# Performance work log

Hardware: AMD Instinct MI355X
Metric: run time of the kernel (lower is better)

Reference implementation:

```python
import jax, jax.numpy as jnp
import numpy as np

B, S, E = 2, 2048, 2048
H, HKV, D = 32, 8, 64  # n_heads, n_kv_heads, head_dim


def _rope(x, cos, sin):
    # x: [B,S,h,D]; cos/sin: [1,S,1,D//2]. Complex rotate on (even,odd) pairs.
    xp = x.reshape(*x.shape[:-1], D // 2, 2)
    x0, x1 = xp[..., 0], xp[..., 1]
    r0 = x0 * cos - x1 * sin
    r1 = x0 * sin + x1 * cos
    return jnp.stack([r0, r1], axis=-1).reshape(x.shape)


def setup_inputs() -> dict:
    key = jax.random.key(0)
    ks = jax.random.split(key, 8)
    sc = 0.02
    # real RoPE frequencies (theta=10000) for realism
    inv = 1.0 / (10000.0 ** (np.arange(0, D, 2, dtype=np.float32) / D))
    t = np.arange(S, dtype=np.float32)
    ang = np.outer(t, inv)  # [S, D/2]
    return {
        "x": jax.random.normal(ks[0], (B, S, E), jnp.float32),
        "start_pos": 0,
        "freqs_cos": jnp.asarray(np.cos(ang))[None, :, None, :],
        "freqs_sin": jnp.asarray(np.sin(ang))[None, :, None, :],
        "wq": jax.random.normal(ks[1], (E, H * D), jnp.float32) * sc,
        "wk": jax.random.normal(ks[2], (E, HKV * D), jnp.float32) * sc,
        "wv": jax.random.normal(ks[3], (E, HKV * D), jnp.float32) * sc,
        "out_w": jax.random.normal(ks[4], (H * D, E), jnp.float32) * sc,
        "out_b": jnp.zeros((E,), jnp.float32),
        "k_cache": jnp.zeros((B, S, HKV, D), jnp.float32),
        "v_cache": jnp.zeros((B, S, HKV, D), jnp.float32),
    }


def reference(x, start_pos, freqs_cos, freqs_sin, wq, wk, wv, out_w, out_b, k_cache, v_cache):
    b, s, _ = x.shape
    q = (x @ wq).reshape(b, s, H, D)
    k = (x @ wk).reshape(b, s, HKV, D)
    v = (x @ wv).reshape(b, s, HKV, D)
    q = _rope(q, freqs_cos[:, :s], freqs_sin[:, :s])
    k = _rope(k, freqs_cos[:, :s], freqs_sin[:, :s])
    # KV-cache append (torch code detaches before writing)
    k_cache = jax.lax.dynamic_update_slice(k_cache, jax.lax.stop_gradient(k), (0, start_pos, 0, 0))
    v_cache = jax.lax.dynamic_update_slice(v_cache, jax.lax.stop_gradient(v), (0, start_pos, 0, 0))
    keys = k_cache[:b, : start_pos + s]    # [b, T, HKV, D]
    values = v_cache[:b, : start_pos + s]
    g = H // HKV
    if g > 1:  # GQA head repeat
        keys = jnp.repeat(keys, g, axis=2)     # [b, T, H, D]
        values = jnp.repeat(values, g, axis=2)
    scores = jnp.einsum("bqhd,bkhd->bhqk", q, keys) / jnp.sqrt(jnp.float32(D))
    att = jax.nn.softmax(scores, axis=-1)  # NOTE: source applies no causal mask
    o = jnp.einsum("bhqk,bkhd->bqhd", att, values).reshape(b, s, H * D)
    return o @ out_w + out_b
```

## Files before the change

kernel.cpp:

```cpp
#include <hip/hip_runtime.h>
#include <math.h>

#define B_    2
#define S_    2048
#define E_    2048
#define H_    32
#define HKV_  8
#define D_    64

typedef __bf16 bf16x8 __attribute__((ext_vector_type(8)));
typedef float  f32x4  __attribute__((ext_vector_type(4)));
typedef float  f32x16 __attribute__((ext_vector_type(16)));
typedef unsigned int u32x2 __attribute__((ext_vector_type(2)));
typedef unsigned int u32x4 __attribute__((ext_vector_type(4)));

#define GPTR(x) ((const __attribute__((address_space(1))) void*)(x))
#define LPTR(x) ((__attribute__((address_space(3))) void*)(x))

#define QK_SCALE_LOG2E 0.18033688011112042f

__global__ __launch_bounds__(256) void convert_kernel(
    const float* __restrict__ in, __bf16* __restrict__ out, int n8)
{
    const int i = blockIdx.x * 256 + threadIdx.x;
    if (i >= n8) return;
    const float4 a = ((const float4*)in)[i * 2];
    const float4 b = ((const float4*)in)[i * 2 + 1];
    bf16x8 o;
    o[0] = (__bf16)a.x; o[1] = (__bf16)a.y; o[2] = (__bf16)a.z; o[3] = (__bf16)a.w;
    o[4] = (__bf16)b.x; o[5] = (__bf16)b.y; o[6] = (__bf16)b.z; o[7] = (__bf16)b.w;
    ((bf16x8*)out)[i] = o;
}

__global__ __launch_bounds__(256) void transpose_convert_all_kernel(
    const float* __restrict__ wq, const float* __restrict__ wk,
    const float* __restrict__ wv, const float* __restrict__ wo,
    __bf16* __restrict__ wT, __bf16* __restrict__ woT)
{
    const float* in; __bf16* out; int N, xb;
    const int x = blockIdx.x;
    if (x < 64)      { in = wq; out = wT;                        N = 2048; xb = x; }
    else if (x < 80) { in = wk; out = wT + (size_t)2048 * 2048;  N = 512;  xb = x - 64; }
    else if (x < 96) { in = wv; out = wT + (size_t)2560 * 2048;  N = 512;  xb = x - 80; }
    else             { in = wo; out = woT;                       N = 2048; xb = x - 96; }
    const int K = 2048;

    __shared__ float tile[32][33];
    const int k0 = blockIdx.y * 32, n0 = xb * 32;
    const int r  = threadIdx.x >> 3;
    const int c4 = (threadIdx.x & 7) * 4;
    const float4 v = *(const float4*)&in[(size_t)(k0 + r) * N + n0 + c4];
    tile[r][c4 + 0] = v.x; tile[r][c4 + 1] = v.y;
    tile[r][c4 + 2] = v.z; tile[r][c4 + 3] = v.w;
    __syncthreads();
    ushort4 o;
    __bf16 h0 = (__bf16)tile[c4 + 0][r]; o.x = __builtin_bit_cast(unsigned short, h0);
    __bf16 h1 = (__bf16)tile[c4 + 1][r]; o.y = __builtin_bit_cast(unsigned short, h1);
    __bf16 h2 = (__bf16)tile[c4 + 2][r]; o.z = __builtin_bit_cast(unsigned short, h2);
    __bf16 h3 = (__bf16)tile[c4 + 3][r]; o.w = __builtin_bit_cast(unsigned short, h3);
    *(ushort4*)&out[(size_t)(n0 + r) * K + k0 + c4] = o;
}

__device__ __forceinline__ void gemm_mfma_body(
    const __bf16* __restrict__ A, const __bf16* __restrict__ Bt,
    int m0, int n0, int K, __bf16* sA, __bf16* sB, f32x4 acc[4][4])
{
    const int t    = threadIdx.x;
    const int w    = t >> 6;
    const int lane = t & 63;
    const int col  = lane & 15;
    const int quad = lane >> 4;
    const int wrow = (w >> 1) * 64;
    const int wcol = (w & 1) * 64;

    const int row0 = t >> 3;
    const int c0   = t & 7;

    for (int k0 = 0; k0 < K; k0 += 64) {
#pragma unroll
        for (int it = 0; it < 4; ++it) {
            const int row  = it * 32 + row0;
            const int csrc = c0 ^ (row & 7);
            __builtin_amdgcn_global_load_lds(
                GPTR(A + (size_t)(m0 + row) * K + k0 + csrc * 8),
                LPTR(sA + (it * 256 + t) * 8), 16, 0, 0);
        }
#pragma unroll
        for (int it = 0; it < 4; ++it) {
            const int row  = it * 32 + row0;
            const int csrc = c0 ^ (row & 7);
            __builtin_amdgcn_global_load_lds(
                GPTR(Bt + (size_t)(n0 + row) * K + k0 + csrc * 8),
                LPTR(sB + (it * 256 + t) * 8), 16, 0, 0);
        }
        __syncthreads();

#pragma unroll
        for (int kk = 0; kk < 2; ++kk) {
            bf16x8 af[4], bfr[4];
#pragma unroll
            for (int i = 0; i < 4; ++i) {
                const int m = wrow + i * 16 + col;
                af[i] = *(const bf16x8*)&sA[m * 64 + (((kk * 4 + quad) ^ (m & 7)) * 8)];
            }
#pragma unroll
            for (int j = 0; j < 4; ++j) {
                const int n = wcol + j * 16 + col;
                bfr[j] = *(const bf16x8*)&sB[n * 64 + (((kk * 4 + quad) ^ (n & 7)) * 8)];
            }
#pragma unroll
            for (int i = 0; i < 4; ++i)
#pragma unroll
                for (int j = 0; j < 4; ++j)
                    acc[i][j] = __builtin_amdgcn_mfma_f32_16x16x32_bf16(
                        af[i], bfr[j], acc[i][j], 0, 0, 0);
        }
        __syncthreads();
    }
}

__global__ __launch_bounds__(256) void gemm_qkv_kernel(
    const __bf16* __restrict__ xb, const __bf16* __restrict__ wT,
    const float* __restrict__ fc, const float* __restrict__ fs,
    __bf16* __restrict__ qb, __bf16* __restrict__ kb, __bf16* __restrict__ vb)
{
    __shared__ __bf16 sA[128 * 64];
    __shared__ __bf16 sB[128 * 64];
    f32x4 acc[4][4];
#pragma unroll
    for (int i = 0; i < 4; ++i)
#pragma unroll
        for (int j = 0; j < 4; ++j) acc[i][j] = (f32x4){0.f, 0.f, 0.f, 0.f};

    const int lin     = blockIdx.y * 24 + blockIdx.x;
    const int logical = (lin & 7) * 96 + (lin >> 3);
    const int bx      = logical % 24;
    const int m0      = (logical / 24) * 128;

    gemm_mfma_body(xb, wT, m0, bx * 128, E_, sA, sB, acc);

    __bf16* Cp; int ldc, nb;
    if (bx < 16)      { Cp = qb; ldc = H_ * D_;   nb = bx * 128; }
    else if (bx < 20) { Cp = kb; ldc = HKV_ * D_; nb = (bx - 16) * 128; }
    else              { Cp = vb; ldc = HKV_ * D_; nb = (bx - 20) * 128; }

    const bool  doRope = (bx < 20);
    const float qsc    = (bx < 16) ? QK_SCALE_LOG2E : 1.0f;

    const int lane = threadIdx.x & 63;
    const int col  = lane & 15;
    const int quad = lane >> 4;
    const int wrow = ((threadIdx.x >> 6) >> 1) * 64;
    const int wcol = ((threadIdx.x >> 6) & 1) * 64;
#pragma unroll
    for (int i = 0; i < 4; ++i)
#pragma unroll
        for (int j = 0; j < 4; ++j)
#pragma unroll
            for (int r = 0; r < 4; ++r) {
                const int m = m0 + wrow + i * 16 + quad * 4 + r;
                const int n = nb + wcol + j * 16 + col;
                float val = acc[i][j][r] * qsc;
                if (doRope) {
                    const int   s    = m & (S_ - 1);
                    const int   pair = (n & 63) >> 1;
                    const float c    = fc[s * 32 + pair];
                    const float sn   = fs[s * 32 + pair];
                    const float oth  = __shfl_xor(val, 1);
                    val = (lane & 1) ? (oth * sn + val * c)
                                     : (val * c - oth * sn);
                }
                Cp[(size_t)m * ldc + n] = (__bf16)val;
            }
}

__global__ __launch_bounds__(256) void gemm_out_kernel(
    const __bf16* __restrict__ ob, const __bf16* __restrict__ woT,
    const float* __restrict__ bias, float* __restrict__ out)
{
    __shared__ __bf16 sA[128 * 64];
    __shared__ __bf16 sB[128 * 64];
    f32x4 acc[4][4];
#pragma unroll
    for (int i = 0; i < 4; ++i)
#pragma unroll
        for (int j = 0; j < 4; ++j) acc[i][j] = (f32x4){0.f, 0.f, 0.f, 0.f};

    const int lin     = blockIdx.y * 16 + blockIdx.x;
    const int logical = (lin & 7) * 64 + (lin >> 3);
    const int n0      = (logical % 16) * 128;
    const int m0      = (logical / 16) * 128;

    gemm_mfma_body(ob, woT, m0, n0, H_ * D_, sA, sB, acc);

    const int lane = threadIdx.x & 63;
    const int col  = lane & 15;
    const int quad = lane >> 4;
    const int wrow = ((threadIdx.x >> 6) >> 1) * 64;
    const int wcol = ((threadIdx.x >> 6) & 1) * 64;
#pragma unroll
    for (int i = 0; i < 4; ++i)
#pragma unroll
        for (int j = 0; j < 4; ++j)
#pragma unroll
            for (int r = 0; r < 4; ++r) {
                const int m = m0 + wrow + i * 16 + quad * 4 + r;
                const int n = n0 + wcol + j * 16 + col;
                out[(size_t)m * E_ + n] = acc[i][j][r] + bias[n];
            }
}

struct StageRegs {
    bf16x8  k0, k1;
    ushort4 va0, vc0, va1, vc1;
};

__device__ __forceinline__ void stage_load(
    StageRegs& r, const __bf16* kbase, const __bf16* vbase, int j0,
    int kkey, int kd, int vkp, int vdg)
{
    const int KSTR = HKV_ * D_;
    const __bf16* kr = kbase + (size_t)(j0 + kkey) * KSTR + kd;
    r.k0 = ((const bf16x8*)kr)[0];
    r.k1 = ((const bf16x8*)kr)[1];
    const __bf16* v0 = vbase + (size_t)(j0 + vkp) * KSTR + vdg;
    r.va0 = *(const ushort4*)(v0);
    r.vc0 = *(const ushort4*)(v0 + KSTR);
    r.va1 = *(const ushort4*)(v0 + 32);
    r.vc1 = *(const ushort4*)(v0 + KSTR + 32);
}

__device__ __forceinline__ void stage_write(
    const StageRegs& r, __bf16 (*sK)[72], __bf16 (*sVT)[72],
    int kkey, int kd, int vkp, int vdg)
{
    *(bf16x8*)&sK[kkey][kd]     = r.k0;
    *(bf16x8*)&sK[kkey][kd + 8] = r.k1;
    *(unsigned int*)&sVT[vdg + 0][vkp]      = ((unsigned)r.vc0.x << 16) | r.va0.x;
    *(unsigned int*)&sVT[vdg + 1][vkp]      = ((unsigned)r.vc0.y << 16) | r.va0.y;
    *(unsigned int*)&sVT[vdg + 2][vkp]      = ((unsigned)r.vc0.z << 16) | r.va0.z;
    *(unsigned int*)&sVT[vdg + 3][vkp]      = ((unsigned)r.vc0.w << 16) | r.va0.w;
    *(unsigned int*)&sVT[vdg + 32 + 0][vkp] = ((unsigned)r.vc1.x << 16) | r.va1.x;
    *(unsigned int*)&sVT[vdg + 32 + 1][vkp] = ((unsigned)r.vc1.y << 16) | r.va1.y;
    *(unsigned int*)&sVT[vdg + 32 + 2][vkp] = ((unsigned)r.vc1.z << 16) | r.va1.z;
    *(unsigned int*)&sVT[vdg + 32 + 3][vkp] = ((unsigned)r.vc1.w << 16) | r.va1.w;
}

__device__ __forceinline__ bf16x8 pack_pa(const f32x16& p, int i0)
{
    unsigned a0, a1, a2, a3;
    asm("v_cvt_pk_bf16_f32 %0, %1, %2" : "=v"(a0) : "v"(p[i0 + 0]), "v"(p[i0 + 1]));
    asm("v_cvt_pk_bf16_f32 %0, %1, %2" : "=v"(a1) : "v"(p[i0 + 2]), "v"(p[i0 + 3]));
    asm("v_cvt_pk_bf16_f32 %0, %1, %2" : "=v"(a2) : "v"(p[i0 + 4]), "v"(p[i0 + 5]));
    asm("v_cvt_pk_bf16_f32 %0, %1, %2" : "=v"(a3) : "v"(p[i0 + 6]), "v"(p[i0 + 7]));
    const u32x2 s02 = __builtin_amdgcn_permlane32_swap(a0, a2, false, false);
    const u32x2 s13 = __builtin_amdgcn_permlane32_swap(a1, a3, false, false);
    return __builtin_bit_cast(bf16x8, (u32x4){s02[0], s13[0], s02[1], s13[1]});
}

__device__ __forceinline__ void attn_tile(
    const __bf16 (*sK)[72], const __bf16 (*sVT)[72],
    const bf16x8* bQ, int lq, int hi,
    f32x16& O0, f32x16& O1, float& lsum)
{
    bf16x8 pa[4];
#pragma unroll
    for (int kb = 0; kb < 2; ++kb) {
        f32x16 p;
#pragma unroll
        for (int i = 0; i < 16; ++i) p[i] = 0.f;
        __builtin_amdgcn_s_setprio(1);
#pragma unroll
        for (int ks = 0; ks < 4; ++ks) {
            const bf16x8 aK = *(const bf16x8*)&sK[kb * 32 + lq][ks * 16 + hi * 8];
            p = __builtin_amdgcn_mfma_f32_32x32x16_bf16(aK, bQ[ks], p, 0, 0, 0);
        }
        __builtin_amdgcn_s_setprio(0);
        float ps = 0.f;
#pragma unroll
        for (int i = 0; i < 16; ++i) {
            p[i] = __builtin_amdgcn_exp2f(p[i]);
            ps += p[i];
        }
        lsum += ps;
        pa[kb * 2]     = pack_pa(p, 0);
        pa[kb * 2 + 1] = pack_pa(p, 8);
    }
    __builtin_amdgcn_s_setprio(1);
#pragma unroll
    for (int ks = 0; ks < 4; ++ks) {
        const bf16x8 vb0 = *(const bf16x8*)&sVT[lq][ks * 16 + hi * 8];
        const bf16x8 vb1 = *(const bf16x8*)&sVT[32 + lq][ks * 16 + hi * 8];
        O0 = __builtin_amdgcn_mfma_f32_32x32x16_bf16(pa[ks], vb0, O0, 0, 0, 0);
        O1 = __builtin_amdgcn_mfma_f32_32x32x16_bf16(pa[ks], vb1, O1, 0, 0, 0);
    }
    __builtin_amdgcn_s_setprio(0);
}

__global__ __launch_bounds__(256, 3) void attn_kernel(
    const __bf16* __restrict__ qw, const __bf16* __restrict__ kw,
    const __bf16* __restrict__ vw, __bf16* __restrict__ ow)
{
    __shared__ __bf16 sK0[64][72], sVT0[64][72];
    __shared__ __bf16 sK1[64][72], sVT1[64][72];

    const int t    = threadIdx.x;
    const int lane = t & 63;
    const int w    = t >> 6;
    const int lq   = lane & 31;
    const int hi   = lane >> 5;

    const int bh  = blockIdx.y;
    const int b   = bh >> 5;
    const int h   = bh & 31;
    const int kvh = h >> 2;
    const int q0  = blockIdx.x * 128 + w * 32;

    bf16x8 bQ[4];
    {
        const __bf16* qrow = qw + (((size_t)b * S_ + q0 + lq) * H_ + h) * D_;
#pragma unroll
        for (int ks = 0; ks < 4; ++ks)
            bQ[ks] = *(const bf16x8*)(qrow + ks * 16 + hi * 8);
    }

    f32x16 O0, O1;
#pragma unroll
    for (int i = 0; i < 16; ++i) { O0[i] = 0.f; O1[i] = 0.f; }
    float lsum = 0.f;

    const __bf16* kbase = kw + ((size_t)b * S_ * HKV_ + kvh) * D_;
    const __bf16* vbase = vw + ((size_t)b * S_ * HKV_ + kvh) * D_;
    const int kkey = t >> 2,        kd  = (t & 3) * 16;
    const int vkp  = (t & 31) * 2,  vdg = (t >> 5) * 4;

    StageRegs sr;
    stage_load(sr, kbase, vbase, 0, kkey, kd, vkp, vdg);
    stage_write(sr, sK0, sVT0, kkey, kd, vkp, vdg);
    __syncthreads();

#pragma unroll 1
    for (int j0 = 0; j0 < S_; j0 += 128) {
        StageRegs nx;
        stage_load(nx, kbase, vbase, j0 + 64, kkey, kd, vkp, vdg);
        attn_tile(sK0, sVT0, bQ, lq, hi, O0, O1, lsum);
        stage_write(nx, sK1, sVT1, kkey, kd, vkp, vdg);
        __syncthreads();
        if (j0 + 128 < S_)
            stage_load(nx, kbase, vbase, j0 + 128, kkey, kd, vkp, vdg);
        attn_tile(sK1, sVT1, bQ, lq, hi, O0, O1, lsum);
        if (j0 + 128 < S_)
            stage_write(nx, sK0, sVT0, kkey, kd, vkp, vdg);
        __syncthreads();
    }

    lsum += __shfl_xor(lsum, 32);
    const float inv = 1.0f / lsum;

#pragma unroll
    for (int r = 0; r < 16; ++r) {
        const int   qr = (r & 3) + 8 * (r >> 2) + 4 * hi;
        const float li = __shfl(inv, qr);
        __bf16* orow = ow + (((size_t)b * S_ + q0 + qr) * H_ + h) * D_;
        orow[lq]      = (__bf16)(O0[r] * li);
        orow[32 + lq] = (__bf16)(O1[r] * li);
    }
}

extern "C" void kernel_launch(void* const* d_in, const int* in_sizes, int n_in,
                              void* d_out, int out_size, void* d_ws, size_t ws_size,
                              hipStream_t stream)
{
    const float* x  = (const float*)d_in[0];
    const float* fc = (const float*)d_in[2];
    const float* fs = (const float*)d_in[3];
    const float* wq = (const float*)d_in[4];
    const float* wk = (const float*)d_in[5];
    const float* wv = (const float*)d_in[6];
    const float* wo = (const float*)d_in[7];
    const float* obias = (const float*)d_in[8];
    float* out = (float*)d_out;

    __bf16* ws  = (__bf16*)d_ws;
    __bf16* xb  = ws;
    __bf16* wT  = xb  + (size_t)4096 * 2048;
    __bf16* woT = wT  + (size_t)3072 * 2048;
    __bf16* qb  = woT + (size_t)2048 * 2048;
    __bf16* kb  = qb  + (size_t)B_ * S_ * H_ * D_;
    __bf16* vb  = kb  + (size_t)B_ * S_ * HKV_ * D_;
    __bf16* obf = vb  + (size_t)B_ * S_ * HKV_ * D_;

    convert_kernel<<<4096, 256, 0, stream>>>(x, xb, 4096 * 2048 / 8);
    transpose_convert_all_kernel<<<dim3(160, 64), 256, 0, stream>>>(
        wq, wk, wv, wo, wT, woT);

    gemm_qkv_kernel<<<dim3(24, 32), 256, 0, stream>>>(xb, wT, fc, fs, qb, kb, vb);

    attn_kernel<<<dim3(S_ / 128, B_ * H_), 256, 0, stream>>>(qb, kb, vb, obf);

    gemm_out_kernel<<<dim3(16, 32), 256, 0, stream>>>(obf, woT, obias, out);
}
```

Measured before the change: 378.9 us.

## Pipeline GEMMs with 4-stage async LDS buffering and larger 256-row tiles

Replaces the single-buffered GEMM main loop with a 4-slot ring of BK=32 LDS tiles filled by global_load_lds, using explicit vmcnt waits and one barrier per iteration so global loads overlap MFMA work. Tiles grow to 256x256 (QKV) and 256x128 (out projection) with 512-thread blocks, and MFMA sections are wrapped in s_setprio. The QKV grid shrinks to 192 blocks and the out-projection grid to 256. This raises register and LDS pressure and could under-fill the CUs.

```diff
diff --git a/kernel.cpp b/kernel.cpp
--- a/kernel.cpp
+++ b/kernel.cpp
@@ -61,147 +61,195 @@
     *(ushort4*)&out[(size_t)(n0 + r) * K + k0 + c4] = o;
 }
 
-__device__ __forceinline__ void gemm_mfma_body(
+template<int BN> struct PG {
+    static constexpr int BM     = 256;
+    static constexpr int BK     = 32;
+    static constexpr int ASLOT  = BM * BK;
+    static constexpr int BSLOT  = BN * BK;
+    static constexpr int SLOT   = ASLOT + BSLOT;
+    static constexpr int BINSTR = BN / 128;
+    static constexpr int L      = 2 + BINSTR;
+    static constexpr int NJ     = BN / 64;
+};
+
+template<int BN>
+__device__ __forceinline__ void stage_tile(
     const __bf16* __restrict__ A, const __bf16* __restrict__ Bt,
-    int m0, int n0, int K, __bf16* sA, __bf16* sB, f32x4 acc[4][4])
-{
+    int m0, int n0, int K, int T, __bf16* sl, int t, int wbase)
+{
+    using G = PG<BN>;
+    const int k0   = T * G::BK;
+    const int rsub = t >> 2;
+    const int cp   = t & 3;
+#pragma unroll
+    for (int g = 0; g < 2; ++g) {
+        const int row = g * 128 + rsub;
+        const int cl  = cp ^ ((row >> 1) & 3);
+        __builtin_amdgcn_global_load_lds(
+            GPTR(A + (size_t)(m0 + row) * K + k0 + cl * 8),
+            LPTR(sl + (g * 512 + wbase) * 8), 16, 0, 0);
+    }
+#pragma unroll
+    for (int g = 0; g < G::BINSTR; ++g) {
+        const int row = g * 128 + rsub;
+        const int cl  = cp ^ ((row >> 1) & 3);
+        __builtin_amdgcn_global_load_lds(
+            GPTR(Bt + (size_t)(n0 + row) * K + k0 + cl * 8),
+            LPTR(sl + G::ASLOT + (g * 512 + wbase) * 8), 16, 0, 0);
+    }
+}
+
+template<int BN>
+__device__ __forceinline__ void compute_tile(
+    const __bf16* sl, int wrow, int wcol, int col, int quad,
+    f32x4 acc[8][PG<BN>::NJ])
+{
+    using G = PG<BN>;
+    bf16x8 af[8], bfr[G::NJ];
+#pragma unroll
+    for (int i = 0; i < 8; ++i) {
+        const int m = wrow + i * 16 + col;
+        af[i] = *(const bf16x8*)&sl[m * 32 + ((quad ^ ((m >> 1) & 3)) * 8)];
+    }
+#pragma unroll
+    for (int j = 0; j < G::NJ; ++j) {
+        const int n = wcol + j * 16 + col;
+        bfr[j] = *(const bf16x8*)&sl[G::ASLOT + n * 32 + ((quad ^ ((n >> 1) & 3)) * 8)];
+    }
+    __builtin_amdgcn_s_setprio(1);
+#pragma unroll
+    for (int i = 0; i < 8; ++i)
+#pragma unroll
+        for (int j = 0; j < G::NJ; ++j)
+            acc[i][j] = __builtin_amdgcn_mfma_f32_16x16x32_bf16(
+                af[i], bfr[j], acc[i][j], 0, 0, 0);
+    __builtin_amdgcn_s_setprio(0);
+}
+
+template<int BN>
+__device__ __forceinline__ void gemm_pipe_body(
+    const __bf16* __restrict__ A, const __bf16* __restrict__ Bt,
+    int m0, int n0, int K, __bf16* sL, f32x4 acc[8][PG<BN>::NJ])
+{
+    using G = PG<BN>;
+    const int t     = threadIdx.x;
+    const int wbase = t & ~63;
+    const int lane  = t & 63;
+    const int col   = lane & 15;
+    const int quad  = lane >> 4;
+    const int w     = t >> 6;
+    const int wrow  = (w >> 2) * 128;
+    const int wcol  = (w & 3) * (BN / 4);
+    const int NT    = K / G::BK;
+
+    stage_tile<BN>(A, Bt, m0, n0, K, 0, sL + 0 * G::SLOT, t, wbase);
+    stage_tile<BN>(A, Bt, m0, n0, K, 1, sL + 1 * G::SLOT, t, wbase);
+    stage_tile<BN>(A, Bt, m0, n0, K, 2, sL + 2 * G::SLOT, t, wbase);
+
+    int T = 0;
+#pragma unroll 1
+    for (; T < NT - 3; ++T) {
+        asm volatile("s_waitcnt vmcnt(%0)" :: "n"(2 * G::L) : "memory");
+        __builtin_amdgcn_s_barrier();
+        stage_tile<BN>(A, Bt, m0, n0, K, T + 3, sL + ((T + 3) & 3) * G::SLOT, t, wbase);
+        compute_tile<BN>(sL + (T & 3) * G::SLOT, wrow, wcol, col, quad, acc);
+    }
+    asm volatile("s_waitcnt vmcnt(%0)" :: "n"(2 * G::L) : "memory");
+    __builtin_amdgcn_s_barrier();
+    compute_tile<BN>(sL + (T & 3) * G::SLOT, wrow, wcol, col, quad, acc); ++T;
+    asm volatile("s_waitcnt vmcnt(%0)" :: "n"(G::L) : "memory");
+    __builtin_amdgcn_s_barrier();
+    compute_tile<BN>(sL + (T & 3) * G::SLOT, wrow, wcol, col, quad, acc); ++T;
+    asm volatile("s_waitcnt vmcnt(0)" ::: "memory");
+    __builtin_amdgcn_s_barrier();
+    compute_tile<BN>(sL + (T & 3) * G::SLOT, wrow, wcol, col, quad, acc);
+}
+
+__global__ __launch_bounds__(512, 2) void gemm_qkv_kernel(
+    const __bf16* __restrict__ xb, const __bf16* __restrict__ wT,
+    const float* __restrict__ fc, const float* __restrict__ fs,
+    __bf16* __restrict__ qb, __bf16* __restrict__ kb, __bf16* __restrict__ vb)
+{
+    __shared__ __bf16 sL[4 * PG<256>::SLOT];
+    f32x4 acc[8][4];
+#pragma unroll
+    for (int i = 0; i < 8; ++i)
+#pragma unroll
+        for (int j = 0; j < 4; ++j) acc[i][j] = (f32x4){0.f, 0.f, 0.f, 0.f};
+
+    const int lin     = blockIdx.x;
+    const int logical = (lin & 7) * 24 + (lin >> 3);
+    const int bx      = logical % 12;
+    const int m0      = (logical / 12) * 256;
+    const int n0      = bx * 256;
+
+    gemm_pipe_body<256>(xb, wT, m0, n0, E_, sL, acc);
+
+    __bf16* Cp; int ldc, base;
+    if (bx < 8)       { Cp = qb; ldc = H_ * D_;   base = 0;    }
+    else if (bx < 10) { Cp = kb; ldc = HKV_ * D_; base = 2048; }
+    else              { Cp = vb; ldc = HKV_ * D_; base = 2560; }
+    const bool  doRope = (bx < 10);
+    const float qsc    = (bx < 8) ? QK_SCALE_LOG2E : 1.0f;
+
     const int t    = threadIdx.x;
-    const int w    = t >> 6;
     const int lane = t & 63;
     const int col  = lane & 15;
     const int quad = lane >> 4;
-    const int wrow = (w >> 1) * 64;
-    const int wcol = (w & 1) * 64;
-
-    const int row0 = t >> 3;
-    const int c0   = t & 7;
-
-    for (int k0 = 0; k0 < K; k0 += 64) {
-#pragma unroll
-        for (int it = 0; it < 4; ++it) {
-            const int row  = it * 32 + row0;
-            const int csrc = c0 ^ (row & 7);
-            __builtin_amdgcn_global_load_lds(
-                GPTR(A + (size_t)(m0 + row) * K + k0 + csrc * 8),
-                LPTR(sA + (it * 256 + t) * 8), 16, 0, 0);
-        }
-#pragma unroll
-        for (int it = 0; it < 4; ++it) {
-            const int row  = it * 32 + row0;
-            const int csrc = c0 ^ (row & 7);
-            __builtin_amdgcn_global_load_lds(
-                GPTR(Bt + (size_t)(n0 + row) * K + k0 + csrc * 8),
-                LPTR(sB + (it * 256 + t) * 8), 16, 0, 0);
-        }
-        __syncthreads();
-
-#pragma unroll
-        for (int kk = 0; kk < 2; ++kk) {
-            bf16x8 af[4], bfr[4];
-#pragma unroll
-            for (int i = 0; i < 4; ++i) {
-                const int m = wrow + i * 16 + col;
-                af[i] = *(const bf16x8*)&sA[m * 64 + (((kk * 4 + quad) ^ (m & 7)) * 8)];
-            }
-#pragma unroll
-            for (int j = 0; j < 4; ++j) {
-                const int n = wcol + j * 16 + col;
-                bfr[j] = *(const bf16x8*)&sB[n * 64 + (((kk * 4 + quad) ^ (n & 7)) * 8)];
-            }
-#pragma unroll
-            for (int i = 0; i < 4; ++i)
-#pragma unroll
-                for (int j = 0; j < 4; ++j)
-                    acc[i][j] = __builtin_amdgcn_mfma_f32_16x16x32_bf16(
-                        af[i], bfr[j], acc[i][j], 0, 0, 0);
-        }
-        __syncthreads();
-    }
-}
-
-__global__ __launch_bounds__(256) void gemm_qkv_kernel(
-    const __bf16* __restrict__ xb, const __bf16* __restrict__ wT,
-    const float* __restrict__ fc, const float* __restrict__ fs,
-    __bf16* __restrict__ qb, __bf16* __restrict__ kb, __bf16* __restrict__ vb)
-{
-    __shared__ __bf16 sA[128 * 64];
-    __shared__ __bf16 sB[128 * 64];
-    f32x4 acc[4][4];
-#pragma unroll
-    for (int i = 0; i < 4; ++i)
-#pragma unroll
-        for (int j = 0; j < 4; ++j) acc[i][j] = (f32x4){0.f, 0.f, 0.f, 0.f};
-
-    const int lin     = blockIdx.y * 24 + blockIdx.x;
-    const int logical = (lin & 7) * 96 + (lin >> 3);
-    const int bx      = logical % 24;
-    const int m0      = (logical / 24) * 128;
-
-    gemm_mfma_body(xb, wT, m0, bx * 128, E_, sA, sB, acc);
-
-    __bf16* Cp; int ldc, nb;
-    if (bx < 16)      { Cp = qb; ldc = H_ * D_;   nb = bx * 128; }
-    else if (bx < 20) { Cp = kb; ldc = HKV_ * D_; nb = (bx - 16) * 128; }
-    else              { Cp = vb; ldc = HKV_ * D_; nb = (bx - 20) * 128; }
-
-    const bool  doRope = (bx < 20);
-    const float qsc    = (bx < 16) ? QK_SCALE_LOG2E : 1.0f;
-
-    const int lane = threadIdx.x & 63;
-    const int col  = lane & 15;
-    const int quad = lane >> 4;
-    const int wrow = ((threadIdx.x >> 6) >> 1) * 64;
-    const int wcol = ((threadIdx.x >> 6) & 1) * 64;
-#pragma unroll
-    for (int i = 0; i < 4; ++i)
+    const int w    = t >> 6;
+    const int wrow = (w >> 2) * 128;
+    const int wcol = (w & 3) * 64;
+#pragma unroll
+    for (int i = 0; i < 8; ++i)
 #pragma unroll
         for (int j = 0; j < 4; ++j)
 #pragma unroll
             for (int r = 0; r < 4; ++r) {
-                const int m = m0 + wrow + i * 16 + quad * 4 + r;
-                const int n = nb + wcol + j * 16 + col;
+                const int m  = m0 + wrow + i * 16 + quad * 4 + r;
+                const int ng = n0 + wcol + j * 16 + col;
                 float val = acc[i][j][r] * qsc;
                 if (doRope) {
                     const int   s    = m & (S_ - 1);
-                    const int   pair = (n & 63) >> 1;
+                    const int   pair = (ng & 63) >> 1;
                     const float c    = fc[s * 32 + pair];
                     const float sn   = fs[s * 32 + pair];
                     const float oth  = __shfl_xor(val, 1);
                     val = (lane & 1) ? (oth * sn + val * c)
                                      : (val * c - oth * sn);
                 }
-                Cp[(size_t)m * ldc + n] = (__bf16)val;
+                Cp[(size_t)m * ldc + (ng - base)] = (__bf16)val;
             }
 }
 
-__global__ __launch_bounds__(256) void gemm_out_kernel(
+__global__ __launch_bounds__(512, 2) void gemm_out_kernel(
     const __bf16* __restrict__ ob, const __bf16* __restrict__ woT,
     const float* __restrict__ bias, float* __restrict__ out)
 {
-    __shared__ __bf16 sA[128 * 64];
-    __shared__ __bf16 sB[128 * 64];
-    f32x4 acc[4][4];
-#pragma unroll
-    for (int i = 0; i < 4; ++i)
-#pragma unroll
-        for (int j = 0; j < 4; ++j) acc[i][j] = (f32x4){0.f, 0.f, 0.f, 0.f};
-
-    const int lin     = blockIdx.y * 16 + blockIdx.x;
-    const int logical = (lin & 7) * 64 + (lin >> 3);
+    __shared__ __bf16 sL[4 * PG<128>::SLOT];
+    f32x4 acc[8][2];
+#pragma unroll
+    for (int i = 0; i < 8; ++i)
+#pragma unroll
+        for (int j = 0; j < 2; ++j) acc[i][j] = (f32x4){0.f, 0.f, 0.f, 0.f};
+
+    const int lin     = blockIdx.x;
+    const int logical = (lin & 7) * 32 + (lin >> 3);
     const int n0      = (logical % 16) * 128;
-    const int m0      = (logical / 16) * 128;
-
-    gemm_mfma_body(ob, woT, m0, n0, H_ * D_, sA, sB, acc);
-
-    const int lane = threadIdx.x & 63;
+    const int m0      = (logical / 16) * 256;
+
+    gemm_pipe_body<128>(ob, woT, m0, n0, H_ * D_, sL, acc);
+
+    const int t    = threadIdx.x;
+    const int lane = t & 63;
     const int col  = lane & 15;
     const int quad = lane >> 4;
-    const int wrow = ((threadIdx.x >> 6) >> 1) * 64;
-    const int wcol = ((threadIdx.x >> 6) & 1) * 64;
-#pragma unroll
-    for (int i = 0; i < 4; ++i)
-#pragma unroll
-        for (int j = 0; j < 4; ++j)
+    const int w    = t >> 6;
+    const int wrow = (w >> 2) * 128;
+    const int wcol = (w & 3) * 32;
+#pragma unroll
+    for (int i = 0; i < 8; ++i)
+#pragma unroll
+        for (int j = 0; j < 2; ++j)
 #pragma unroll
             for (int r = 0; r < 4; ++r) {
                 const int m = m0 + wrow + i * 16 + quad * 4 + r;
@@ -394,9 +442,9 @@
     transpose_convert_all_kernel<<<dim3(160, 64), 256, 0, stream>>>(
         wq, wk, wv, wo, wT, woT);
 
-    gemm_qkv_kernel<<<dim3(24, 32), 256, 0, stream>>>(xb, wT, fc, fs, qb, kb, vb);
+    gemm_qkv_kernel<<<192, 512, 0, stream>>>(xb, wT, fc, fs, qb, kb, vb);
 
     attn_kernel<<<dim3(S_ / 128, B_ * H_), 256, 0, stream>>>(qb, kb, vb, obf);
 
-    gemm_out_kernel<<<dim3(16, 32), 256, 0, stream>>>(obf, woT, obias, out);
-}
+    gemm_out_kernel<<<256, 512, 0, stream>>>(obf, woT, obias, out);
+}
```

After: 359.3 us. 5.2% less time.
